# Performance work log

Measured on AMD Instinct MI355X. Metric: run time of the kernel, lower is better.

Reference implementation:

```python
import jax, jax.numpy as jnp
import numpy as np

B, R, A, S, SR = 128, 1024, 512, 196, 64


def _linear(x, w, b):
    return x @ w.T + b


def _lstm_cell(x, h, c, wih, whh, bih, bhh):
    # torch.nn.LSTMCell gate order: i, f, g, o
    g = x @ wih.T + bih + h @ whh.T + bhh
    i, f, gg, o = jnp.split(g, 4, axis=-1)
    c2 = jax.nn.sigmoid(f) * c + jax.nn.sigmoid(i) * jnp.tanh(gg)
    h2 = jax.nn.sigmoid(o) * jnp.tanh(c2)
    return h2, c2


def _attention(h, att_feats, p_att, mask, h2att_w, h2att_b, aw, ab):
    att_h = _linear(h, h2att_w, h2att_b)[:, None, :]            # [B,1,A]
    dot = jnp.tanh(p_att + att_h)                               # [B,S,A]
    e = jnp.einsum('bsa,a->bs', dot, aw[0]) + ab[0]             # alpha_net
    w = jax.nn.softmax(e, axis=1)
    w = w * mask
    w = w / jnp.sum(w, axis=1, keepdims=True)
    return jnp.einsum('bs,bsd->bd', w, att_feats)


def setup_inputs() -> dict:
    key = jax.random.key(0)
    ks = iter(jax.random.split(key, 80))
    def rn(shape, scale=1.0):
        return jax.random.normal(next(ks), shape, dtype=jnp.float32) * scale
    w = 0.02  # weight init scale
    inp = {
        'xt': rn((B, R)), 'state_h': rn((2, B, R)), 'state_c': rn((2, B, R)),
        'fc_feats': rn((B, R)),
        'att_feats': rn((B, S, R)), 'obj_feats': rn((B, S, R)),
        'attr_feats': rn((B, S, R)), 'rela_feats': rn((B, SR, R)),
        'p_obj_feats': rn((B, S, A)), 'p_attr_feats': rn((B, S, A)),
        'p_rela_feats': rn((B, SR, A)),
        'att_masks': jnp.ones((B, S), jnp.float32),
        'rela_masks': jnp.ones((B, SR), jnp.float32),
        'att_wih': rn((4*R, 3*R), w), 'att_whh': rn((4*R, R), w),
        'att_bih': rn((4*R,), w), 'att_bhh': rn((4*R,), w),
        'lang_wih': rn((4*R, 4*R), w), 'lang_whh': rn((4*R, R), w),
        'lang_bih': rn((4*R,), w), 'lang_bhh': rn((4*R,), w),
        'xt2_w': rn((R, R), w), 'xt2_b': rn((R,), w),
        'h_att2_w': rn((R, R), w), 'h_att2_b': rn((R,), w),
        'r_i2h_w': rn((R, 4*R), w), 'r_i2h_b': rn((R,), w),
        'r_h2h_w': rn((R, R), w), 'r_h2h_b': rn((R,), w),
        'huu_w': rn((R, 3*R), w), 'huu_b': rn((R,), w),
        'obj_h2att_w': rn((A, R), w), 'obj_h2att_b': rn((A,), w),
        'obj_alpha_w': rn((1, A), w), 'obj_alpha_b': rn((1,), w),
        'attr_h2att_w': rn((A, R), w), 'attr_h2att_b': rn((A,), w),
        'attr_alpha_w': rn((1, A), w), 'attr_alpha_b': rn((1,), w),
        'rela_h2att_w': rn((A, R), w), 'rela_h2att_b': rn((A,), w),
        'rela_alpha_w': rn((1, A), w), 'rela_alpha_b': rn((1,), w),
        'fr_lin_w': rn((R, R), w), 'fr_lin_b': rn((R,), w),
        'fr_emb_w': rn((R, R), w), 'fr_emb_b': rn((R,), w),
        'ho_lin_w': rn((R, R), w), 'ho_lin_b': rn((R,), w),
        'ho_emb_w': rn((R, R), w), 'ho_emb_b': rn((R,), w),
        'ada_alpha_w': rn((1, R), w), 'ada_alpha_b': rn((1,), w),
        'cfe_w': rn((R, A), w), 'cfe_b': rn((R,), w),
    }
    return inp


def reference(xt, state_h, state_c, fc_feats, att_feats, obj_feats, attr_feats,
              rela_feats, p_obj_feats, p_attr_feats, p_rela_feats, att_masks,
              rela_masks, att_wih, att_whh, att_bih, att_bhh, lang_wih,
              lang_whh, lang_bih, lang_bhh, xt2_w, xt2_b, h_att2_w, h_att2_b,
              r_i2h_w, r_i2h_b, r_h2h_w, r_h2h_b, huu_w, huu_b, obj_h2att_w,
              obj_h2att_b, obj_alpha_w, obj_alpha_b, attr_h2att_w,
              attr_h2att_b, attr_alpha_w, attr_alpha_b, rela_h2att_w,
              rela_h2att_b, rela_alpha_w, rela_alpha_b, fr_lin_w, fr_lin_b,
              fr_emb_w, fr_emb_b, ho_lin_w, ho_lin_b, ho_emb_w, ho_emb_b,
              ada_alpha_w, ada_alpha_b, cfe_w, cfe_b):
    # eval mode: all dropouts are identity
    prev_h = state_h[1]
    att_in = jnp.concatenate([prev_h, fc_feats, xt], axis=1)            # [B,3R]
    h_att_raw, c_att = _lstm_cell(att_in, state_h[0], state_c[0],
                                  att_wih, att_whh, att_bih, att_bhh)
    h_att = _linear(xt, xt2_w, xt2_b) + _linear(h_att_raw, h_att2_w, h_att2_b)
    att_obj = _attention(h_att, obj_feats, p_obj_feats, att_masks,
                         obj_h2att_w, obj_h2att_b, obj_alpha_w, obj_alpha_b)
    att_attr = _attention(h_att, attr_feats, p_attr_feats, att_masks,
                          attr_h2att_w, attr_h2att_b, attr_alpha_w, attr_alpha_b)
    att_rela = _attention(h_att, rela_feats, p_rela_feats, rela_masks,
                          rela_h2att_w, rela_h2att_b, rela_alpha_w, rela_alpha_b)
    lang_in = jnp.concatenate([h_att, att_obj, att_attr, att_rela], axis=1)  # [B,4R]
    h_lang, c_lang = _lstm_cell(lang_in, state_h[1], state_c[1],
                                lang_wih, lang_whh, lang_bih, lang_bhh)
    tanh_mt = jnp.tanh(c_lang)
    n5 = _linear(lang_in, r_i2h_w, r_i2h_b) + _linear(state_h[1], r_h2h_w, r_h2h_b)
    st = jax.nn.sigmoid(n5) * tanh_mt                                    # [B,R]
    # AdaAtt_attention(h_lang, st, att_feats, p_obj_feats)
    cfe = _linear(p_obj_feats, cfe_w, cfe_b)                             # [B,S,R]
    fake_region = jax.nn.relu(_linear(st, fr_lin_w, fr_lin_b))           # [B,R]
    fr_embed = _linear(fake_region, fr_emb_w, fr_emb_b)
    ho = jnp.tanh(_linear(h_lang, ho_lin_w, ho_lin_b))
    ho_embed = _linear(ho, ho_emb_w, ho_emb_b)
    img_all = jnp.concatenate([fake_region[:, None, :], att_feats], axis=1)    # [B,S+1,R]
    img_all_embed = jnp.concatenate([fr_embed[:, None, :], cfe], axis=1)
    hA = jnp.tanh(img_all_embed + ho_embed[:, None, :])
    e = jnp.einsum('bsr,r->bs', hA, ada_alpha_w[0]) + ada_alpha_b[0]
    PI = jax.nn.softmax(e, axis=1)                                       # [B,S+1]
    visAtt = jnp.einsum('bs,bsd->bd', PI, img_all)
    beta = PI[:, -1:]
    c_t_hat = beta * fake_region + (1.0 - beta) * visAtt
    output = _linear(jnp.concatenate([h_att, h_lang, c_t_hat], axis=1), huu_w, huu_b)
    new_h = jnp.stack([h_att, h_lang])
    new_c = jnp.stack([c_att, c_lang])
    return output, new_h, new_c
```

## Files before the change

### kernel.cpp

```cpp
#include <hip/hip_runtime.h>
#include <cstddef>

#define B 128
#define R 1024

typedef __attribute__((ext_vector_type(8))) short short8;
typedef __attribute__((ext_vector_type(4))) float f32x4;

__device__ __forceinline__ float sigf(float x) { return 1.0f / (1.0f + __expf(-x)); }

__device__ __forceinline__ short f2bf(float f) {
    unsigned int u = __float_as_uint(f);
    u += 0x7fff + ((u >> 16) & 1);
    return (short)(u >> 16);
}

__device__ __forceinline__ short8 cvt8(float4 u, float4 v) {
    short8 r;
    r[0] = f2bf(u.x); r[1] = f2bf(u.y); r[2] = f2bf(u.z); r[3] = f2bf(u.w);
    r[4] = f2bf(v.x); r[5] = f2bf(v.y); r[6] = f2bf(v.z); r[7] = f2bf(v.w);
    return r;
}

__device__ __forceinline__ void gll16(const void* g, void* l) {
    __builtin_amdgcn_global_load_lds(
        (const __attribute__((address_space(1))) unsigned int*)g,
        (__attribute__((address_space(3))) unsigned int*)l, 16, 0, 0);
}

struct GJob {
    const float* A1; const float* A2; const float* A3;
    const float* W1; const float* W2; const float* W3;
    float* C;
    int lda1, lda2, lda3;
    int ldw1, ldw2, ldw3;
    int K1, K12, Ktot;
    int ldc, Kchunk, nb;
};

__global__ __launch_bounds__(256) void gemm_sk_kernel(GJob j0, GJob j1, GJob j2, int njobs)
{
    GJob j = j0;
    int nbx = blockIdx.x;
    if (njobs > 1 && nbx >= j.nb) { nbx -= j.nb; j = j1; }
    if (njobs > 2 && nbx >= j.nb) { nbx -= j.nb; j = j2; }

    const int bn   = nbx * 64;
    const int kbeg = blockIdx.y * j.Kchunk;
    const int kend = kbeg + j.Kchunk;

    __shared__ short sA[128 * 40];
    __shared__ short sB[64 * 40];
    const int tid  = threadIdx.x;
    const int rA   = tid >> 1;
    const int kha  = (tid & 1) << 4;
    const int rB   = tid >> 2;
    const int khb  = (tid & 3) << 3;
    const int lane = tid & 63;
    const int wid  = tid >> 6;
    const int wm   = wid * 32;
    const int fr_  = lane & 15;
    const int kof  = (lane >> 4) * 8;

    f32x4 acc[2][4];
#pragma unroll
    for (int m = 0; m < 2; ++m)
#pragma unroll
        for (int n = 0; n < 4; ++n)
            acc[m][n] = (f32x4)0.0f;

    for (int k0 = kbeg; k0 < kend; k0 += 32) {
        int kgA = k0 + kha;
        const float* pa;
        if (kgA < j.K1)       pa = j.A1 + (size_t)rA * j.lda1 + kgA;
        else if (kgA < j.K12) pa = j.A2 + (size_t)rA * j.lda2 + (kgA - j.K1);
        else                  pa = j.A3 + (size_t)rA * j.lda3 + (kgA - j.K12);
        int kgB = k0 + khb;
        const float* pw;
        if (kgB < j.K1)       pw = j.W1 + (size_t)(bn + rB) * j.ldw1 + kgB;
        else if (kgB < j.K12) pw = j.W2 + (size_t)(bn + rB) * j.ldw2 + (kgB - j.K1);
        else                  pw = j.W3 + (size_t)(bn + rB) * j.ldw3 + (kgB - j.K12);

        float4 a0 = ((const float4*)pa)[0];
        float4 a1 = ((const float4*)pa)[1];
        float4 a2 = ((const float4*)pa)[2];
        float4 a3 = ((const float4*)pa)[3];
        float4 w0 = ((const float4*)pw)[0];
        float4 w1 = ((const float4*)pw)[1];
        __syncthreads();
        *(short8*)&sA[rA * 40 + kha]     = cvt8(a0, a1);
        *(short8*)&sA[rA * 40 + kha + 8] = cvt8(a2, a3);
        *(short8*)&sB[rB * 40 + khb]     = cvt8(w0, w1);
        __syncthreads();
        short8 af[2], bf[4];
#pragma unroll
        for (int m = 0; m < 2; ++m)
            af[m] = *(const short8*)&sA[(wm + m * 16 + fr_) * 40 + kof];
#pragma unroll
        for (int n = 0; n < 4; ++n)
            bf[n] = *(const short8*)&sB[(n * 16 + fr_) * 40 + kof];
#pragma unroll
        for (int m = 0; m < 2; ++m)
#pragma unroll
            for (int n = 0; n < 4; ++n)
                acc[m][n] = __builtin_amdgcn_mfma_f32_16x16x32_bf16(af[m], bf[n], acc[m][n], 0, 0, 0);
    }

#pragma unroll
    for (int m = 0; m < 2; ++m) {
        int row0 = wm + m * 16 + ((lane >> 4) << 2);
#pragma unroll
        for (int n = 0; n < 4; ++n) {
            int col = bn + n * 16 + fr_;
#pragma unroll
            for (int rg = 0; rg < 4; ++rg)
                atomicAdd(&j.C[(size_t)(row0 + rg) * j.ldc + col], acc[m][n][rg]);
        }
    }
}

__global__ __launch_bounds__(256) void prologue_kernel(
    float* __restrict__ ws, int nws, float* __restrict__ o, const float* __restrict__ bias,
    const float* __restrict__ ph, const float* __restrict__ fc, const float* __restrict__ xt,
    float* __restrict__ att_in,
    const float* __restrict__ P, const float* __restrict__ W,
    short* __restrict__ Pbf, short* __restrict__ Wbf, int ZB)
{
    int blk = blockIdx.x;
    int tid = threadIdx.x;
    if (blk < ZB) {
        int idx = blk * 256 + tid;
        if (idx < nws) ws[idx] = 0.0f;
        else if (idx < nws + 131072) { int i = idx - nws; o[i] = bias[i & 1023]; }
        return;
    }
    blk -= ZB;
    if (blk < 384) {
        int idx = blk * 256 + tid;
        int r = idx / 768, c4 = idx - r * 768;
        int col = c4 * 4;
        const float* src = (col < 1024) ? (ph + (size_t)r * 1024 + col)
                         : (col < 2048) ? (fc + (size_t)r * 1024 + col - 1024)
                                        : (xt + (size_t)r * 1024 + col - 2048);
        *(float4*)(att_in + (size_t)r * 3072 + col) = *(const float4*)src;
        return;
    }
    blk -= 384;
    int lane = tid & 63;
    int fr = lane & 15, kg = lane >> 4;
    if (blk < 6272) {
        int w = blk * 4 + (tid >> 6);
        int rt = w >> 4, ks = w & 15;
        const float* src = P + (size_t)(rt * 16 + fr) * 512 + ks * 32 + kg * 8;
        float4 u = ((const float4*)src)[0];
        float4 v = ((const float4*)src)[1];
        *(short8*)(Pbf + ((size_t)w * 64 + lane) * 8) = cvt8(u, v);
    } else {
        int w = (blk - 6272) * 4 + (tid >> 6);
        int ct = w >> 4, ks = w & 15;
        const float* src = W + (size_t)(ct * 16 + fr) * 512 + ks * 32 + kg * 8;
        float4 u = ((const float4*)src)[0];
        float4 v = ((const float4*)src)[1];
        *(short8*)(Wbf + ((size_t)w * 64 + lane) * 8) = cvt8(u, v);
    }
}

__global__ __launch_bounds__(256) void cfe_v7_kernel(
    const short* __restrict__ Pbf, const short* __restrict__ Wbf,
    const float* __restrict__ cb, const float* __restrict__ hoe,
    const float* __restrict__ ho_b, const float* __restrict__ aw,
    float* __restrict__ e)
{
    int p = blockIdx.x;
    int x8 = p & 7, rest = p >> 3;
    int n8 = rest & 7, q = rest >> 3;
    int m = q * 8 + x8;
    if (m >= 196) return;
    const int bm = m * 128, bn = n8 * 128;

    __shared__ short sA[2][8 * 512];
    __shared__ short sB[2][8 * 512];

    const int tid  = threadIdx.x;
    const int lane = tid & 63;
    const int wid  = tid >> 6;
    const int wm   = (wid >> 1) * 64;
    const int wn   = (wid & 1) * 64;
    const int fr_  = lane & 15;
    const int rtbA = bm >> 4;
    const int rtbB = bn >> 4;

    auto STAGE = [&](int buf, int ks) {
#pragma unroll
        for (int jj = 0; jj < 4; ++jj) {
            int fid = wid * 4 + jj;
            int rt  = fid & 7;
            if (fid < 8) {
                const short* src = Pbf + ((size_t)((rtbA + rt) * 16 + ks) * 64 + lane) * 8;
                gll16(src, &sA[buf][rt * 512]);
            } else {
                const short* src = Wbf + ((size_t)((rtbB + rt) * 16 + ks) * 64 + lane) * 8;
                gll16(src, &sB[buf][rt * 512]);
            }
        }
    };

    f32x4 acc[4][4];
#pragma unroll
    for (int mi = 0; mi < 4; ++mi)
#pragma unroll
        for (int n = 0; n < 4; ++n)
            acc[mi][n] = (f32x4)0.0f;

    STAGE(0, 0);
    for (int r = 0; r < 16; ++r) {
        const int buf = r & 1;
        __syncthreads();
        if (r < 15) STAGE(buf ^ 1, r + 1);
        short8 af[4], bf8[4];
#pragma unroll
        for (int mi = 0; mi < 4; ++mi)
            af[mi] = *(const short8*)&sA[buf][((wm >> 4) + mi) * 512 + lane * 8];
#pragma unroll
        for (int n = 0; n < 4; ++n)
            bf8[n] = *(const short8*)&sB[buf][((wn >> 4) + n) * 512 + lane * 8];
#pragma unroll
        for (int mi = 0; mi < 4; ++mi)
#pragma unroll
            for (int n = 0; n < 4; ++n)
                acc[mi][n] = __builtin_amdgcn_mfma_f32_16x16x32_bf16(af[mi], bf8[n], acc[mi][n], 0, 0, 0);
        __syncthreads();
    }

    const int l4 = lane >> 4;
    const int rbase = bm + wm + (l4 << 2);
    const int b0 = rbase / 196;
    const int b1 = (rbase + 51) / 196;
    float cba[4], awa[4], hv0[4], hv1[4];
#pragma unroll
    for (int n = 0; n < 4; ++n) {
        int col = bn + wn + n * 16 + fr_;
        cba[n] = cb[col] + ho_b[col];
        awa[n] = aw[col];
        hv0[n] = hoe[(size_t)b0 * R + col];
        hv1[n] = hoe[(size_t)b1 * R + col];
    }
#pragma unroll
    for (int mi = 0; mi < 4; ++mi) {
#pragma unroll
        for (int rg = 0; rg < 4; ++rg) {
            int gr = rbase + mi * 16 + rg;
            int bb = gr / 196;
            bool second = (bb != b0);
            float part = 0.0f;
#pragma unroll
            for (int n = 0; n < 4; ++n) {
                float hv = second ? hv1[n] : hv0[n];
                part += tanhf(acc[mi][n][rg] + cba[n] + hv) * awa[n];
            }
            part += __shfl_xor(part, 1);
            part += __shfl_xor(part, 2);
            part += __shfl_xor(part, 4);
            part += __shfl_xor(part, 8);
            if (fr_ == 0)
                atomicAdd(&e[bb * 197 + 1 + (gr - bb * 196)], part);
        }
    }
}

__global__ __launch_bounds__(256) void cfe_fallback_kernel(
    const float* __restrict__ P, const float* __restrict__ Wf,
    const float* __restrict__ cb, const float* __restrict__ hoe,
    const float* __restrict__ ho_b, const float* __restrict__ aw,
    float* __restrict__ e)
{
    int p = blockIdx.x;
    int x8 = p & 7, rest = p >> 3;
    int n8 = rest & 7, q = rest >> 3;
    int m = q * 8 + x8;
    if (m >= 196) return;
    const int bm = m * 128, bn = n8 * 128;

    __shared__ short sA[128 * 72];
    __shared__ short sB[128 * 72];
    const int tid  = threadIdx.x;
    const int lane = tid & 63;
    const int wid  = tid >> 6;
    const int wm   = (wid >> 1) * 64;
    const int wn   = (wid & 1) * 64;
    const int fr_  = lane & 15;
    const int kof  = (lane >> 4) * 8;

    f32x4 acc[4][4];
#pragma unroll
    for (int mi = 0; mi < 4; ++mi)
#pragma unroll
        for (int n = 0; n < 4; ++n)
            acc[mi][n] = (f32x4)0.0f;

    for (int k0 = 0; k0 < 512; k0 += 64) {
        __syncthreads();
        int row = tid >> 1;
        int half = (tid & 1) * 32;
        const float* pa = P + (size_t)(bm + row) * 512 + k0 + half;
        const float* pw = Wf + (size_t)(bn + row) * 512 + k0 + half;
#pragma unroll
        for (int c = 0; c < 32; c += 8) {
            float4 u = *(const float4*)(pa + c);
            float4 v = *(const float4*)(pa + c + 4);
            *(short8*)&sA[row * 72 + half + c] = cvt8(u, v);
            float4 uw = *(const float4*)(pw + c);
            float4 vw = *(const float4*)(pw + c + 4);
            *(short8*)&sB[row * 72 + half + c] = cvt8(uw, vw);
        }
        __syncthreads();
#pragma unroll
        for (int ks = 0; ks < 64; ks += 32) {
            short8 af[4], bf[4];
#pragma unroll
            for (int mi = 0; mi < 4; ++mi)
                af[mi] = *(const short8*)&sA[(wm + mi * 16 + fr_) * 72 + ks + kof];
#pragma unroll
            for (int n = 0; n < 4; ++n)
                bf[n] = *(const short8*)&sB[(wn + n * 16 + fr_) * 72 + ks + kof];
#pragma unroll
            for (int mi = 0; mi < 4; ++mi)
#pragma unroll
                for (int n = 0; n < 4; ++n)
                    acc[mi][n] = __builtin_amdgcn_mfma_f32_16x16x32_bf16(af[mi], bf[n], acc[mi][n], 0, 0, 0);
        }
    }

    const int l4 = lane >> 4;
    const int rbase = bm + wm + (l4 << 2);
    const int b0 = rbase / 196;
    const int b1 = (rbase + 51) / 196;
    float cba[4], awa[4], hv0[4], hv1[4];
#pragma unroll
    for (int n = 0; n < 4; ++n) {
        int col = bn + wn + n * 16 + fr_;
        cba[n] = cb[col] + ho_b[col];
        awa[n] = aw[col];
        hv0[n] = hoe[(size_t)b0 * R + col];
        hv1[n] = hoe[(size_t)b1 * R + col];
    }
#pragma unroll
    for (int mi = 0; mi < 4; ++mi) {
#pragma unroll
        for (int rg = 0; rg < 4; ++rg) {
            int gr = rbase + mi * 16 + rg;
            int bb = gr / 196;
            bool second = (bb != b0);
            float part = 0.0f;
#pragma unroll
            for (int n = 0; n < 4; ++n) {
                float hv = second ? hv1[n] : hv0[n];
                part += tanhf(acc[mi][n][rg] + cba[n] + hv) * awa[n];
            }
            part += __shfl_xor(part, 1);
            part += __shfl_xor(part, 2);
            part += __shfl_xor(part, 4);
            part += __shfl_xor(part, 8);
            if (fr_ == 0)
                atomicAdd(&e[bb * 197 + 1 + (gr - bb * 196)], part);
        }
    }
}

__global__ __launch_bounds__(256) void lstm_kernel(
    float* __restrict__ g, const float* __restrict__ bih, const float* __restrict__ bhh,
    const float* __restrict__ cprev, float* __restrict__ h, float* __restrict__ c,
    const float* __restrict__ n5, const float* __restrict__ nb1,
    const float* __restrict__ nb2, float* __restrict__ st)
{
    int t = blockIdx.x * 256 + threadIdx.x;
    int b = t >> 8, d4 = (t & 255) * 4;
    float* gr = g + (size_t)b * 4096;
    float4 gi = *(float4*)(gr + d4);
    float4 gf = *(float4*)(gr + 1024 + d4);
    float4 gg = *(float4*)(gr + 2048 + d4);
    float4 go = *(float4*)(gr + 3072 + d4);
    float4 bi1 = *(const float4*)(bih + d4),        bh1 = *(const float4*)(bhh + d4);
    float4 bi2 = *(const float4*)(bih + 1024 + d4), bh2 = *(const float4*)(bhh + 1024 + d4);
    float4 bi3 = *(const float4*)(bih + 2048 + d4), bh3 = *(const float4*)(bhh + 2048 + d4);
    float4 bi4 = *(const float4*)(bih + 3072 + d4), bh4 = *(const float4*)(bhh + 3072 + d4);
    float4 cp = *(const float4*)(cprev + (size_t)b * 1024 + d4);
    float4 zero = {0.f, 0.f, 0.f, 0.f};
    *(float4*)(gr + d4) = zero; *(float4*)(gr + 1024 + d4) = zero;
    *(float4*)(gr + 2048 + d4) = zero; *(float4*)(gr + 3072 + d4) = zero;
    float4 cc, hh;
    float iv, fv, gv, ov, c2, tc;
    iv = sigf(gi.x + bi1.x + bh1.x); fv = sigf(gf.x + bi2.x + bh2.x);
    gv = tanhf(gg.x + bi3.x + bh3.x); ov = sigf(go.x + bi4.x + bh4.x);
    c2 = fv * cp.x + iv * gv; tc = tanhf(c2); cc.x = c2; hh.x = ov * tc;
    float tcx = tc;
    iv = sigf(gi.y + bi1.y + bh1.y); fv = sigf(gf.y + bi2.y + bh2.y);
    gv = tanhf(gg.y + bi3.y + bh3.y); ov = sigf(go.y + bi4.y + bh4.y);
    c2 = fv * cp.y + iv * gv; tc = tanhf(c2); cc.y = c2; hh.y = ov * tc;
    float tcy = tc;
    iv = sigf(gi.z + bi1.z + bh1.z); fv = sigf(gf.z + bi2.z + bh2.z);
    gv = tanhf(gg.z + bi3.z + bh3.z); ov = sigf(go.z + bi4.z + bh4.z);
    c2 = fv * cp.z + iv * gv; tc = tanhf(c2); cc.z = c2; hh.z = ov * tc;
    float tcz = tc;
    iv = sigf(gi.w + bi1.w + bh1.w); fv = sigf(gf.w + bi2.w + bh2.w);
    gv = tanhf(gg.w + bi3.w + bh3.w); ov = sigf(go.w + bi4.w + bh4.w);
    c2 = fv * cp.w + iv * gv; tc = tanhf(c2); cc.w = c2; hh.w = ov * tc;
    float tcw = tc;
    *(float4*)(c + (size_t)b * 1024 + d4) = cc;
    *(float4*)(h + (size_t)b * 1024 + d4) = hh;
    if (st) {
        float4 nv = *(const float4*)(n5 + (size_t)b * 1024 + d4);
        float4 n1 = *(const float4*)(nb1 + d4), n2 = *(const float4*)(nb2 + d4);
        float4 sv;
        sv.x = sigf(nv.x + n1.x + n2.x) * tcx;
        sv.y = sigf(nv.y + n1.y + n2.y) * tcy;
        sv.z = sigf(nv.z + n1.z + n2.z) * tcz;
        sv.w = sigf(nv.w + n1.w + n2.w) * tcw;
        *(float4*)(st + (size_t)b * 1024 + d4) = sv;
    }
}

__global__ __launch_bounds__(256) void hatt_epi_kernel(
    float* __restrict__ lang_in, const float* __restrict__ b1,
    const float* __restrict__ b2, float* __restrict__ h_att_out)
{
    int t = blockIdx.x * 256 + threadIdx.x;
    int r = t >> 8, c4 = (t & 255) * 4;
    float4 v = *(float4*)(lang_in + (size_t)r * 4096 + c4);
    float4 x1 = *(const float4*)(b1 + c4), x2 = *(const float4*)(b2 + c4);
    v.x += x1.x + x2.x; v.y += x1.y + x2.y; v.z += x1.z + x2.z; v.w += x1.w + x2.w;
    *(float4*)(lang_in + (size_t)r * 4096 + c4) = v;
    *(float4*)(h_att_out + (size_t)r * 1024 + c4) = v;
}

__global__ __launch_bounds__(256) void att_e3_kernel(
    const float* __restrict__ p0, const float* __restrict__ p1, const float* __restrict__ p2,
    const float* __restrict__ ah3,
    const float* __restrict__ b0, const float* __restrict__ b1, const float* __restrict__ b2,
    const float* __restrict__ aw0, const float* __restrict__ aw1, const float* __restrict__ aw2,
    float* __restrict__ e3)
{
    int wid = threadIdx.x >> 6, lane = threadIdx.x & 63;
    int idx = blockIdx.x * 4 + wid;
    const float* p; const float* bb; const float* aw; int S, loc, mod;
    if (idx < 25088)      { mod = 0; loc = idx;          p = p0; bb = b0; aw = aw0; S = 196; }
    else if (idx < 50176) { mod = 1; loc = idx - 25088;  p = p1; bb = b1; aw = aw1; S = 196; }
    else                  { mod = 2; loc = idx - 50176;  p = p2; bb = b2; aw = aw2; S = 64; }
    int b = loc / S;
    const float4* pr = (const float4*)(p + (size_t)loc * 512);
    const float4* ab = (const float4*)(ah3 + (size_t)mod * 65536 + (size_t)b * 512);
    const float4* bb4 = (const float4*)bb;
    const float4* aw4 = (const float4*)aw;
    float sum = 0.0f;
#pragma unroll
    for (int k = 0; k < 2; ++k) {
        int a = k * 64 + lane;
        float4 pv = pr[a], av = ab[a], bv = bb4[a], wv = aw4[a];
        sum += tanhf(pv.x + av.x + bv.x) * wv.x;
        sum += tanhf(pv.y + av.y + bv.y) * wv.y;
        sum += tanhf(pv.z + av.z + bv.z) * wv.z;
        sum += tanhf(pv.w + av.w + bv.w) * wv.w;
    }
#pragma unroll
    for (int off = 32; off; off >>= 1) sum += __shfl_down(sum, off);
    if (lane == 0) e3[idx] = sum;
}

__global__ __launch_bounds__(256) void softmax3_kernel(
    float* __restrict__ e3, const float* __restrict__ am, const float* __restrict__ rm)
{
    __shared__ float red[256];
    int mod = blockIdx.x >> 7, b = blockIdx.x & 127, tid = threadIdx.x;
    int S = (mod == 2) ? 64 : 196;
    float* e = e3 + ((mod == 0) ? 0 : (mod == 1) ? 25088 : 50176) + (size_t)b * S;
    const float* mask = ((mod == 2) ? rm : am) + (size_t)b * S;
    float v = (tid < S) ? e[tid] : -3.4e38f;
    red[tid] = v; __syncthreads();
    for (int s = 128; s; s >>= 1) { if (tid < s) red[tid] = fmaxf(red[tid], red[tid + s]); __syncthreads(); }
    float m = red[0]; __syncthreads();
    float p = (tid < S) ? __expf(v - m) : 0.0f;
    red[tid] = p; __syncthreads();
    for (int s = 128; s; s >>= 1) { if (tid < s) red[tid] += red[tid + s]; __syncthreads(); }
    float s1 = red[0]; __syncthreads();
    float w = (tid < S) ? (p / s1) * mask[tid] : 0.0f;
    red[tid] = w; __syncthreads();
    for (int s = 128; s; s >>= 1) { if (tid < s) red[tid] += red[tid + s]; __syncthreads(); }
    float s2 = red[0];
    if (tid < S) e[tid] = w / s2;
}

__global__ __launch_bounds__(256) void wsum3_kernel(
    const float* __restrict__ e3,
    const float* __restrict__ f0, const float* __restrict__ f1, const float* __restrict__ f2,
    float* __restrict__ lang_in)
{
    int mod = blockIdx.x >> 7;
    int idx = (blockIdx.x & 127) * 256 + threadIdx.x;
    int b = idx >> 8, d4 = idx & 255;
    int S = (mod == 2) ? 64 : 196;
    int Sq = (S + 3) >> 2;
    int s0 = blockIdx.y * Sq, s1 = min(S, s0 + Sq);
    const float4* f = (const float4*)(((mod == 0) ? f0 : (mod == 1) ? f1 : f2) + ((size_t)b * S) * R) + d4;
    const float* wb = e3 + ((mod == 0) ? 0 : (mod == 1) ? 25088 : 50176) + (size_t)b * S;
    float4 acc = {0.f, 0.f, 0.f, 0.f};
#pragma unroll 4
    for (int s = s0; s < s1; ++s) {
        float w = wb[s];
        float4 fv = f[(size_t)s * 256];
        acc.x = fmaf(w, fv.x, acc.x); acc.y = fmaf(w, fv.y, acc.y);
        acc.z = fmaf(w, fv.z, acc.z); acc.w = fmaf(w, fv.w, acc.w);
    }
    float* dst = lang_in + (size_t)b * 4096 + 1024 + mod * 1024 + d4 * 4;
    atomicAdd(dst + 0, acc.x); atomicAdd(dst + 1, acc.y);
    atomicAdd(dst + 2, acc.z); atomicAdd(dst + 3, acc.w);
}

__global__ __launch_bounds__(256) void relutanh_kernel(
    float* __restrict__ fr, const float* __restrict__ frb,
    float* __restrict__ ho, const float* __restrict__ hob,
    float* __restrict__ ct_acc)
{
    int idx = blockIdx.x * 256 + threadIdx.x;
    int c = idx & 1023;
    if (idx < 131072) { fr[idx] = fmaxf(fr[idx] + frb[c], 0.0f); ct_acc[idx] = 0.0f; }
    else { int i = idx - 131072; ho[i] = tanhf(ho[i] + hob[c]); }
}

__global__ __launch_bounds__(256) void softmax_ada_kernel(
    float* __restrict__ e,
    const float* __restrict__ fre, const float* __restrict__ frb,
    const float* __restrict__ hoe, const float* __restrict__ hob,
    const float* __restrict__ aw)
{
    __shared__ float red[256];
    int b = blockIdx.x, tid = threadIdx.x;
    float s = 0.0f;
#pragma unroll
    for (int k = 0; k < 4; ++k) {
        int r = k * 256 + tid;
        s += tanhf(fre[(size_t)b * R + r] + frb[r] + hoe[(size_t)b * R + r] + hob[r]) * aw[r];
    }
    red[tid] = s; __syncthreads();
    for (int t = 128; t; t >>= 1) { if (tid < t) red[tid] += red[tid + t]; __syncthreads(); }
    float e0 = red[0]; __syncthreads();
    float v = (tid == 0) ? e0 : ((tid < 197) ? e[(size_t)b * 197 + tid] : -3.4e38f);
    red[tid] = v; __syncthreads();
    for (int t = 128; t; t >>= 1) { if (tid < t) red[tid] = fmaxf(red[tid], red[tid + t]); __syncthreads(); }
    float m = red[0]; __syncthreads();
    float p = (tid < 197) ? __expf(v - m) : 0.0f;
    red[tid] = p; __syncthreads();
    for (int t = 128; t; t >>= 1) { if (tid < t) red[tid] += red[tid + t]; __syncthreads(); }
    float s1 = red[0];
    if (tid < 197) e[(size_t)b * 197 + tid] = p / s1;
}

__global__ __launch_bounds__(256) void ct_part_kernel(
    const float* __restrict__ PI, const float* __restrict__ attf,
    float* __restrict__ ct_acc)
{
    int b = blockIdx.x, d4 = threadIdx.x;
    int s0 = blockIdx.y * 14, s1 = min(196, s0 + 14);
    const float* pb = PI + b * 197;
    const float4* af = (const float4*)(attf + ((size_t)b * 196) * R) + d4;
    float4 acc = {0.f, 0.f, 0.f, 0.f};
#pragma unroll 2
    for (int s = s0; s < s1; ++s) {
        float w = pb[1 + s];
        float4 av = af[(size_t)s * 256];
        acc.x = fmaf(w, av.x, acc.x); acc.y = fmaf(w, av.y, acc.y);
        acc.z = fmaf(w, av.z, acc.z); acc.w = fmaf(w, av.w, acc.w);
    }
    float* dst = ct_acc + (size_t)b * 1024 + d4 * 4;
    atomicAdd(dst + 0, acc.x); atomicAdd(dst + 1, acc.y);
    atomicAdd(dst + 2, acc.z); atomicAdd(dst + 3, acc.w);
}

__global__ __launch_bounds__(256) void ct_fin_kernel(
    const float* __restrict__ PI, const float* __restrict__ fr,
    const float* __restrict__ ct_acc, float* __restrict__ ct)
{
    int idx = blockIdx.x * 256 + threadIdx.x;
    int b = idx >> 10;
    const float* pb = PI + b * 197;
    float f = fr[idx];
    float acc = pb[0] * f + ct_acc[idx];
    float beta = pb[196];
    ct[idx] = beta * f + (1.0f - beta) * acc;
}

extern "C" void kernel_launch(void* const* d_in, const int* in_sizes, int n_in,
                              void* d_out, int out_size, void* d_ws, size_t ws_size,
                              hipStream_t stream)
{
    const float* xt         = (const float*)d_in[0];
    const float* state_h    = (const float*)d_in[1];
    const float* state_c    = (const float*)d_in[2];
    const float* fc_feats   = (const float*)d_in[3];
    const float* att_feats  = (const float*)d_in[4];
    const float* obj_feats  = (const float*)d_in[5];
    const float* attr_feats = (const float*)d_in[6];
    const float* rela_feats = (const float*)d_in[7];
    const float* p_obj      = (const float*)d_in[8];
    const float* p_attr     = (const float*)d_in[9];
    const float* p_rela     = (const float*)d_in[10];
    const float* att_masks  = (const float*)d_in[11];
    const float* rela_masks = (const float*)d_in[12];
    const float* att_wih    = (const float*)d_in[13];
    const float* att_whh    = (const float*)d_in[14];
    const float* att_bih    = (const float*)d_in[15];
    const float* att_bhh    = (const float*)d_in[16];
    const float* lang_wih   = (const float*)d_in[17];
    const float* lang_whh   = (const float*)d_in[18];
    const float* lang_bih   = (const float*)d_in[19];
    const float* lang_bhh   = (const float*)d_in[20];
    const float* xt2_w      = (const float*)d_in[21];
    const float* xt2_b      = (const float*)d_in[22];
    const float* h_att2_w   = (const float*)d_in[23];
    const float* h_att2_b   = (const float*)d_in[24];
    const float* r_i2h_w    = (const float*)d_in[25];
    const float* r_i2h_b    = (const float*)d_in[26];
    const float* r_h2h_w    = (const float*)d_in[27];
    const float* r_h2h_b    = (const float*)d_in[28];
    const float* huu_w      = (const float*)d_in[29];
    const float* huu_b      = (const float*)d_in[30];
    const float* obj_h2att_w  = (const float*)d_in[31];
    const float* obj_h2att_b  = (const float*)d_in[32];
    const float* obj_alpha_w  = (const float*)d_in[33];
    const float* attr_h2att_w = (const float*)d_in[35];
    const float* attr_h2att_b = (const float*)d_in[36];
    const float* attr_alpha_w = (const float*)d_in[37];
    const float* rela_h2att_w = (const float*)d_in[39];
    const float* rela_h2att_b = (const float*)d_in[40];
    const float* rela_alpha_w = (const float*)d_in[41];
    const float* fr_lin_w   = (const float*)d_in[43];
    const float* fr_lin_b   = (const float*)d_in[44];
    const float* fr_emb_w   = (const float*)d_in[45];
    const float* fr_emb_b   = (const float*)d_in[46];
    const float* ho_lin_w   = (const float*)d_in[47];
    const float* ho_lin_b   = (const float*)d_in[48];
    const float* ho_emb_w   = (const float*)d_in[49];
    const float* ho_emb_b   = (const float*)d_in[50];
    const float* ada_w      = (const float*)d_in[51];
    const float* cfe_w      = (const float*)d_in[53];
    const float* cfe_b      = (const float*)d_in[54];

    float* out = (float*)d_out;
    float* wsf = (float*)d_ws;

    float* g        = wsf + 0;
    float* lang_in  = wsf + 524288;
    float* att_h3   = wsf + 1048576;
    float* n5       = wsf + 1245184;
    float* fr       = wsf + 1376256;
    float* fre      = wsf + 1507328;
    float* ho       = wsf + 1638400;
    float* hoe      = wsf + 1769472;
    float* e_ada    = wsf + 1900544;
    const int NATOM = 1926144;
    float* att_in    = wsf + 1926144;
    float* ct_acc    = att_in;
    float* h_att_raw = wsf + 2319360;
    float* e3        = wsf + 2450432;
    float* st        = wsf + 2527232;
    float* ct        = wsf + 2658304;
    short* Pbf       = (short*)(wsf + 2789376);
    short* Wbf       = Pbf + 12845056;
    const bool big = ws_size >= (size_t)2789376 * 4 + (size_t)13369344 * 2;

    float* h_att_out  = out + 131072;
    float* h_lang_out = out + 262144;
    float* c_att_out  = out + 393216;
    float* c_lang_out = out + 524288;

    const float* prev_h = state_h + 131072;

    GJob Z = {};
    auto mk = [&](const float* A1, int lda1, int K1, const float* W1, int ldw1,
                  float* C, int ldc, int N, int Ktot, int Kchunk) {
        GJob j = Z;
        j.A1 = A1; j.lda1 = lda1; j.K1 = K1; j.K12 = Ktot; j.Ktot = Ktot;
        j.W1 = W1; j.ldw1 = ldw1;
        j.C = C; j.ldc = ldc; j.Kchunk = Kchunk; j.nb = N / 64;
        return j;
    };

    {
        const int ZB = (NATOM + 131072) / 256;
        int grid = ZB + 384 + (big ? 6528 : 0);
        prologue_kernel<<<grid, 256, 0, stream>>>(wsf, NATOM, out, huu_b,
            prev_h, fc_feats, xt, att_in, p_obj, cfe_w, Pbf, Wbf, ZB);
    }

    {
        GJob j = mk(att_in, 3072, 3072, att_wih, 3072, g, 4096, 4096, 4096, 512);
        j.A2 = state_h; j.lda2 = 1024; j.W2 = att_whh; j.ldw2 = 1024; j.K12 = 4096;
        gemm_sk_kernel<<<dim3(64, 8), 256, 0, stream>>>(j, Z, Z, 1);
    }
    lstm_kernel<<<128, 256, 0, stream>>>(g, att_bih, att_bhh, state_c, h_att_raw, c_att_out,
                                         nullptr, nullptr, nullptr, nullptr);

    {
        GJob j = mk(xt, 1024, 1024, xt2_w, 1024, lang_in, 4096, 1024, 2048, 128);
        j.A2 = h_att_raw; j.lda2 = 1024; j.W2 = h_att2_w; j.ldw2 = 1024; j.K12 = 2048;
        gemm_sk_kernel<<<dim3(16, 16), 256, 0, stream>>>(j, Z, Z, 1);
    }
    hatt_epi_kernel<<<128, 256, 0, stream>>>(lang_in, xt2_b, h_att2_b, h_att_out);

    {
        GJob j0 = mk(lang_in, 4096, 1024, obj_h2att_w,  1024, att_h3 + 0,      512, 512, 1024, 64);
        GJob j1 = mk(lang_in, 4096, 1024, attr_h2att_w, 1024, att_h3 + 65536,  512, 512, 1024, 64);
        GJob j2 = mk(lang_in, 4096, 1024, rela_h2att_w, 1024, att_h3 + 131072, 512, 512, 1024, 64);
        gemm_sk_kernel<<<dim3(24, 16), 256, 0, stream>>>(j0, j1, j2, 3);
    }
    att_e3_kernel<<<14592, 256, 0, stream>>>(p_obj, p_attr, p_rela, att_h3,
        obj_h2att_b, attr_h2att_b, rela_h2att_b, obj_alpha_w, attr_alpha_w, rela_alpha_w, e3);
    softmax3_kernel<<<384, 256, 0, stream>>>(e3, att_masks, rela_masks);
    wsum3_kernel<<<dim3(384, 4), 256, 0, stream>>>(e3, obj_feats, attr_feats, rela_feats, lang_in);

    {
        GJob j0 = mk(lang_in, 4096, 4096, lang_wih, 4096, g, 4096, 4096, 5120, 640);
        j0.A2 = prev_h; j0.lda2 = 1024; j0.W2 = lang_whh; j0.ldw2 = 1024; j0.K12 = 5120;
        GJob j1 = mk(lang_in, 4096, 4096, r_i2h_w, 4096, n5, 1024, 1024, 5120, 640);
        j1.A2 = prev_h; j1.lda2 = 1024; j1.W2 = r_h2h_w; j1.ldw2 = 1024; j1.K12 = 5120;
        gemm_sk_kernel<<<dim3(80, 8), 256, 0, stream>>>(j0, j1, Z, 2);
    }
    lstm_kernel<<<128, 256, 0, stream>>>(g, lang_bih, lang_bhh, state_c + 131072,
                                         h_lang_out, c_lang_out, n5, r_i2h_b, r_h2h_b, st);

    {
        GJob j0 = mk(st, 1024, 1024, fr_lin_w, 1024, fr, 1024, 1024, 1024, 64);
        GJob j1 = mk(h_lang_out, 1024, 1024, ho_lin_w, 1024, ho, 1024, 1024, 1024, 64);
        gemm_sk_kernel<<<dim3(32, 16), 256, 0, stream>>>(j0, j1, Z, 2);
    }
    relutanh_kernel<<<1024, 256, 0, stream>>>(fr, fr_lin_b, ho, ho_lin_b, ct_acc);

    {
        GJob j0 = mk(fr, 1024, 1024, fr_emb_w, 1024, fre, 1024, 1024, 1024, 64);
        GJob j1 = mk(ho, 1024, 1024, ho_emb_w, 1024, hoe, 1024, 1024, 1024, 64);
        gemm_sk_kernel<<<dim3(32, 16), 256, 0, stream>>>(j0, j1, Z, 2);
    }
    if (big) {
        cfe_v7_kernel<<<1600, 256, 0, stream>>>(Pbf, Wbf, cfe_b, hoe, ho_emb_b, ada_w, e_ada);
    } else {
        cfe_fallback_kernel<<<1600, 256, 0, stream>>>(p_obj, cfe_w, cfe_b, hoe, ho_emb_b, ada_w, e_ada);
    }
    softmax_ada_kernel<<<128, 256, 0, stream>>>(e_ada, fre, fr_emb_b, hoe, ho_emb_b, ada_w);
    ct_part_kernel<<<dim3(128, 14), 256, 0, stream>>>(e_ada, att_feats, ct_acc);
    ct_fin_kernel<<<512, 256, 0, stream>>>(e_ada, fr, ct_acc, ct);

    {
        GJob j = mk(lang_in, 4096, 1024, huu_w, 3072, out, 1024, 1024, 3072, 192);
        j.A2 = h_lang_out; j.lda2 = 1024; j.W2 = huu_w + 1024; j.ldw2 = 3072; j.K12 = 2048;
        j.A3 = ct; j.lda3 = 1024; j.W3 = huu_w + 2048; j.ldw3 = 3072;
        gemm_sk_kernel<<<dim3(16, 16), 256, 0, stream>>>(j, Z, Z, 1);
    }

    (void)in_sizes; (void)n_in; (void)out_size; (void)ws_size;
}
```

Measured before the change: 407.8 us.

## Double-buffer split-K GEMM and fuse bias+activation into A-operand load

The split-K GEMM now uses double-buffered LDS, prefetching the next K tile into registers while MFMAs run on the current one, with one barrier per iteration. The separate relu/tanh bias kernel is removed. Bias and activation are applied while loading the A operand of the embedding GEMMs, and the relu is recomputed in ct_fin. ct_acc moves to its own slice of the workspace so it can be zeroed with the other atomic targets, since the removed kernel used to clear it. A trailing barrier in the cfe kernel loop is also dropped, which may rely on the next iteration's barrier for safety. The cost is tanhf being evaluated redundantly in each block that loads the same A rows.

New measurement: 388.3 us, median of 3. 4.8% less time.

```diff
diff --git a/kernel.cpp b/kernel.cpp
--- a/kernel.cpp
+++ b/kernel.cpp
@@ -31,11 +31,12 @@
 struct GJob {
     const float* A1; const float* A2; const float* A3;
     const float* W1; const float* W2; const float* W3;
+    const float* abias;
     float* C;
     int lda1, lda2, lda3;
     int ldw1, ldw2, ldw3;
     int K1, K12, Ktot;
-    int ldc, Kchunk, nb;
+    int ldc, Kchunk, nb, aact;
 };
 
 __global__ __launch_bounds__(256) void gemm_sk_kernel(GJob j0, GJob j1, GJob j2, int njobs)
@@ -47,10 +48,9 @@
 
     const int bn   = nbx * 64;
     const int kbeg = blockIdx.y * j.Kchunk;
-    const int kend = kbeg + j.Kchunk;
-
-    __shared__ short sA[128 * 40];
-    __shared__ short sB[64 * 40];
+
+    __shared__ short sA[2][128 * 40];
+    __shared__ short sB[2][64 * 40];
     const int tid  = threadIdx.x;
     const int rA   = tid >> 1;
     const int kha  = (tid & 1) << 4;
@@ -62,48 +62,81 @@
     const int fr_  = lane & 15;
     const int kof  = (lane >> 4) * 8;
 
-    f32x4 acc[2][4];
-#pragma unroll
-    for (int m = 0; m < 2; ++m)
-#pragma unroll
-        for (int n = 0; n < 4; ++n)
-            acc[m][n] = (f32x4)0.0f;
-
-    for (int k0 = kbeg; k0 < kend; k0 += 32) {
+    float4 a0, a1, a2, a3, w0, w1;
+    auto LOAD = [&](int k0) {
         int kgA = k0 + kha;
         const float* pa;
         if (kgA < j.K1)       pa = j.A1 + (size_t)rA * j.lda1 + kgA;
         else if (kgA < j.K12) pa = j.A2 + (size_t)rA * j.lda2 + (kgA - j.K1);
         else                  pa = j.A3 + (size_t)rA * j.lda3 + (kgA - j.K12);
+        a0 = ((const float4*)pa)[0];
+        a1 = ((const float4*)pa)[1];
+        a2 = ((const float4*)pa)[2];
+        a3 = ((const float4*)pa)[3];
+        if (j.aact) {
+            float4 b0 = *(const float4*)(j.abias + kgA);
+            float4 b1 = *(const float4*)(j.abias + kgA + 4);
+            float4 b2 = *(const float4*)(j.abias + kgA + 8);
+            float4 b3 = *(const float4*)(j.abias + kgA + 12);
+            a0.x += b0.x; a0.y += b0.y; a0.z += b0.z; a0.w += b0.w;
+            a1.x += b1.x; a1.y += b1.y; a1.z += b1.z; a1.w += b1.w;
+            a2.x += b2.x; a2.y += b2.y; a2.z += b2.z; a2.w += b2.w;
+            a3.x += b3.x; a3.y += b3.y; a3.z += b3.z; a3.w += b3.w;
+            if (j.aact == 1) {
+                a0.x = fmaxf(a0.x, 0.f); a0.y = fmaxf(a0.y, 0.f); a0.z = fmaxf(a0.z, 0.f); a0.w = fmaxf(a0.w, 0.f);
+                a1.x = fmaxf(a1.x, 0.f); a1.y = fmaxf(a1.y, 0.f); a1.z = fmaxf(a1.z, 0.f); a1.w = fmaxf(a1.w, 0.f);
+                a2.x = fmaxf(a2.x, 0.f); a2.y = fmaxf(a2.y, 0.f); a2.z = fmaxf(a2.z, 0.f); a2.w = fmaxf(a2.w, 0.f);
+                a3.x = fmaxf(a3.x, 0.f); a3.y = fmaxf(a3.y, 0.f); a3.z = fmaxf(a3.z, 0.f); a3.w = fmaxf(a3.w, 0.f);
+            } else {
+                a0.x = tanhf(a0.x); a0.y = tanhf(a0.y); a0.z = tanhf(a0.z); a0.w = tanhf(a0.w);
+                a1.x = tanhf(a1.x); a1.y = tanhf(a1.y); a1.z = tanhf(a1.z); a1.w = tanhf(a1.w);
+                a2.x = tanhf(a2.x); a2.y = tanhf(a2.y); a2.z = tanhf(a2.z); a2.w = tanhf(a2.w);
+                a3.x = tanhf(a3.x); a3.y = tanhf(a3.y); a3.z = tanhf(a3.z); a3.w = tanhf(a3.w);
+            }
+        }
         int kgB = k0 + khb;
         const float* pw;
         if (kgB < j.K1)       pw = j.W1 + (size_t)(bn + rB) * j.ldw1 + kgB;
         else if (kgB < j.K12) pw = j.W2 + (size_t)(bn + rB) * j.ldw2 + (kgB - j.K1);
         else                  pw = j.W3 + (size_t)(bn + rB) * j.ldw3 + (kgB - j.K12);
-
-        float4 a0 = ((const float4*)pa)[0];
-        float4 a1 = ((const float4*)pa)[1];
-        float4 a2 = ((const float4*)pa)[2];
-        float4 a3 = ((const float4*)pa)[3];
-        float4 w0 = ((const float4*)pw)[0];
-        float4 w1 = ((const float4*)pw)[1];
-        __syncthreads();
-        *(short8*)&sA[rA * 40 + kha]     = cvt8(a0, a1);
-        *(short8*)&sA[rA * 40 + kha + 8] = cvt8(a2, a3);
-        *(short8*)&sB[rB * 40 + khb]     = cvt8(w0, w1);
-        __syncthreads();
+        w0 = ((const float4*)pw)[0];
+        w1 = ((const float4*)pw)[1];
+    };
+    auto WRITE = [&](int buf) {
+        *(short8*)&sA[buf][rA * 40 + kha]     = cvt8(a0, a1);
+        *(short8*)&sA[buf][rA * 40 + kha + 8] = cvt8(a2, a3);
+        *(short8*)&sB[buf][rB * 40 + khb]     = cvt8(w0, w1);
+    };
+
+    f32x4 acc[2][4];
+#pragma unroll
+    for (int m = 0; m < 2; ++m)
+#pragma unroll
+        for (int n = 0; n < 4; ++n)
+            acc[m][n] = (f32x4)0.0f;
+
+    LOAD(kbeg);
+    WRITE(0);
+    __syncthreads();
+    const int nr = j.Kchunk >> 5;
+    for (int r = 0; r < nr; ++r) {
+        const int buf = r & 1;
+        const bool more = (r + 1 < nr);
+        if (more) LOAD(kbeg + (r + 1) * 32);
         short8 af[2], bf[4];
 #pragma unroll
         for (int m = 0; m < 2; ++m)
-            af[m] = *(const short8*)&sA[(wm + m * 16 + fr_) * 40 + kof];
+            af[m] = *(const short8*)&sA[buf][(wm + m * 16 + fr_) * 40 + kof];
 #pragma unroll
         for (int n = 0; n < 4; ++n)
-            bf[n] = *(const short8*)&sB[(n * 16 + fr_) * 40 + kof];
+            bf[n] = *(const short8*)&sB[buf][(n * 16 + fr_) * 40 + kof];
 #pragma unroll
         for (int m = 0; m < 2; ++m)
 #pragma unroll
             for (int n = 0; n < 4; ++n)
                 acc[m][n] = __builtin_amdgcn_mfma_f32_16x16x32_bf16(af[m], bf[n], acc[m][n], 0, 0, 0);
+        if (more) WRITE(buf ^ 1);
+        __syncthreads();
     }
 
 #pragma unroll
@@ -229,7 +262,6 @@
 #pragma unroll
             for (int n = 0; n < 4; ++n)
                 acc[mi][n] = __builtin_amdgcn_mfma_f32_16x16x32_bf16(af[mi], bf8[n], acc[mi][n], 0, 0, 0);
-        __syncthreads();
     }
 
     const int l4 = lane >> 4;
@@ -515,17 +547,6 @@
     atomicAdd(dst + 2, acc.z); atomicAdd(dst + 3, acc.w);
 }
 
-__global__ __launch_bounds__(256) void relutanh_kernel(
-    float* __restrict__ fr, const float* __restrict__ frb,
-    float* __restrict__ ho, const float* __restrict__ hob,
-    float* __restrict__ ct_acc)
-{
-    int idx = blockIdx.x * 256 + threadIdx.x;
-    int c = idx & 1023;
-    if (idx < 131072) { fr[idx] = fmaxf(fr[idx] + frb[c], 0.0f); ct_acc[idx] = 0.0f; }
-    else { int i = idx - 131072; ho[i] = tanhf(ho[i] + hob[c]); }
-}
-
 __global__ __launch_bounds__(256) void softmax_ada_kernel(
     float* __restrict__ e,
     const float* __restrict__ fre, const float* __restrict__ frb,
@@ -576,13 +597,14 @@
 }
 
 __global__ __launch_bounds__(256) void ct_fin_kernel(
-    const float* __restrict__ PI, const float* __restrict__ fr,
-    const float* __restrict__ ct_acc, float* __restrict__ ct)
+    const float* __restrict__ PI, const float* __restrict__ fr_raw,
+    const float* __restrict__ frb, const float* __restrict__ ct_acc,
+    float* __restrict__ ct)
 {
     int idx = blockIdx.x * 256 + threadIdx.x;
-    int b = idx >> 10;
+    int b = idx >> 10, c = idx & 1023;
     const float* pb = PI + b * 197;
-    float f = fr[idx];
+    float f = fmaxf(fr_raw[idx] + frb[c], 0.0f);
     float acc = pb[0] * f + ct_acc[idx];
     float beta = pb[196];
     ct[idx] = beta * f + (1.0f - beta) * acc;
@@ -656,16 +678,16 @@
     float* ho       = wsf + 1638400;
     float* hoe      = wsf + 1769472;
     float* e_ada    = wsf + 1900544;
-    const int NATOM = 1926144;
-    float* att_in    = wsf + 1926144;
-    float* ct_acc    = att_in;
-    float* h_att_raw = wsf + 2319360;
-    float* e3        = wsf + 2450432;
-    float* st        = wsf + 2527232;
-    float* ct        = wsf + 2658304;
-    short* Pbf       = (short*)(wsf + 2789376);
+    float* ct_acc   = wsf + 1926144;
+    const int NATOM = 2057216;
+    float* att_in    = wsf + 2057216;
+    float* h_att_raw = wsf + 2450432;
+    float* e3        = wsf + 2581504;
+    float* st        = wsf + 2658304;
+    float* ct        = wsf + 2789376;
+    short* Pbf       = (short*)(wsf + 2920448);
     short* Wbf       = Pbf + 12845056;
-    const bool big = ws_size >= (size_t)2789376 * 4 + (size_t)13369344 * 2;
+    const bool big = ws_size >= (size_t)2920448 * 4 + (size_t)13369344 * 2;
 
     float* h_att_out  = out + 131072;
     float* h_lang_out = out + 262144;
@@ -732,11 +754,11 @@
         GJob j1 = mk(h_lang_out, 1024, 1024, ho_lin_w, 1024, ho, 1024, 1024, 1024, 64);
         gemm_sk_kernel<<<dim3(32, 16), 256, 0, stream>>>(j0, j1, Z, 2);
     }
-    relutanh_kernel<<<1024, 256, 0, stream>>>(fr, fr_lin_b, ho, ho_lin_b, ct_acc);
-
     {
         GJob j0 = mk(fr, 1024, 1024, fr_emb_w, 1024, fre, 1024, 1024, 1024, 64);
+        j0.abias = fr_lin_b; j0.aact = 1;
         GJob j1 = mk(ho, 1024, 1024, ho_emb_w, 1024, hoe, 1024, 1024, 1024, 64);
+        j1.abias = ho_lin_b; j1.aact = 2;
         gemm_sk_kernel<<<dim3(32, 16), 256, 0, stream>>>(j0, j1, Z, 2);
     }
     if (big) {
@@ -746,7 +768,7 @@
     }
     softmax_ada_kernel<<<128, 256, 0, stream>>>(e_ada, fre, fr_emb_b, hoe, ho_emb_b, ada_w);
     ct_part_kernel<<<dim3(128, 14), 256, 0, stream>>>(e_ada, att_feats, ct_acc);
-    ct_fin_kernel<<<512, 256, 0, stream>>>(e_ada, fr, ct_acc, ct);
+    ct_fin_kernel<<<512, 256, 0, stream>>>(e_ada, fr, fr_lin_b, ct_acc, ct);
 
     {
         GJob j = mk(lang_in, 4096, 1024, huu_w, 3072, out, 1024, 1024, 3072, 192);
```
